# Kernel tuning notes

Hardware: AMD Instinct MI355X
Metric: run time of the kernel (lower is better)

## Reference

```python
import jax, jax.numpy as jnp
import numpy as np

MIN_NORM = 1e-15
BALL_EPS = 1e-5  # projection margin for the Poincare ball


def _tanh(x):
    return jnp.tanh(jnp.clip(x, -15.0, 15.0))


def _artanh(x):
    return jnp.arctanh(jnp.clip(x, -1.0 + 1e-5, 1.0 - 1e-5))


def givens_rotations(r, x):
    # r, x: (N, d) with d even -> (N, d)
    g = r.reshape(r.shape[0], -1, 2)
    g = g / jnp.maximum(jnp.linalg.norm(g, axis=-1, keepdims=True), MIN_NORM)
    xp = x.reshape(x.shape[0], -1, 2)
    swap = jnp.concatenate([-xp[..., 1:], xp[..., :1]], axis=-1)
    return (g[..., :1] * xp + g[..., 1:] * swap).reshape(r.shape[0], -1)


def givens_reflection(r, x):
    g = r.reshape(r.shape[0], -1, 2)
    g = g / jnp.maximum(jnp.linalg.norm(g, axis=-1, keepdims=True), MIN_NORM)
    xp = x.reshape(x.shape[0], -1, 2)
    a = jnp.concatenate([xp[..., :1], -xp[..., 1:]], axis=-1)
    b = jnp.concatenate([xp[..., 1:], xp[..., :1]], axis=-1)
    return (g[..., :1] * a + g[..., 1:] * b).reshape(r.shape[0], -1)


def expmap0(u, c):
    sqrt_c = jnp.sqrt(c)
    u_norm = jnp.maximum(jnp.linalg.norm(u, axis=-1, keepdims=True), MIN_NORM)
    return _tanh(sqrt_c * u_norm) * u / (sqrt_c * u_norm)


def mobius_add(x, y, c):
    x2 = jnp.sum(x * x, -1, keepdims=True)
    y2 = jnp.sum(y * y, -1, keepdims=True)
    xy = jnp.sum(x * y, -1, keepdims=True)
    num = (1 + 2 * c * xy + c * y2) * x + (1 - c * x2) * y
    denom = 1 + 2 * c * xy + c * c * x2 * y2
    return num / jnp.maximum(denom, MIN_NORM)


def project(x, c):
    norm = jnp.maximum(jnp.linalg.norm(x, axis=-1, keepdims=True), MIN_NORM)
    maxnorm = (1.0 - BALL_EPS) / jnp.sqrt(c)
    return jnp.where(norm > maxnorm, x / norm * maxnorm, x)


def hyp_distance_multi_c_bmm(x, v, c):
    # x: (nc, cs, d) queries; v: (nc, ns, d) candidates; c: (nc, cs, 1) curvatures
    sqrt_c = jnp.sqrt(c)                                              # (nc, cs, 1)
    vnorm = jnp.linalg.norm(v, axis=-1, keepdims=True).transpose(0, 2, 1)  # (nc, 1, ns)
    xv = jnp.einsum('bcd,bnd->bcn', x, v) / vnorm                     # (nc, cs, ns)
    gamma = _tanh(sqrt_c * vnorm) / sqrt_c                            # (nc, cs, ns)
    x2 = jnp.sum(x * x, -1, keepdims=True)                            # (nc, cs, 1)
    c1 = 1 - 2 * c * gamma * xv + c * gamma ** 2
    c2 = 1 - c * x2
    num = jnp.sqrt(jnp.maximum(c1 ** 2 * x2 + c2 ** 2 * gamma ** 2 - 2 * c1 * c2 * gamma * xv, 0.0))
    denom = 1 - 2 * c * gamma * xv + c ** 2 * gamma ** 2 * x2
    dist = _artanh(sqrt_c * num / jnp.maximum(denom, MIN_NORM))
    return 2 * dist / sqrt_c                                          # (nc, cs, ns)


def setup_inputs() -> dict:
    key = jax.random.key(0)
    nc, cs, ns, d = 16, 1024, 1024, 512
    B = nc * cs
    ks = jax.random.split(key, 8)
    return {
        'head': jax.random.normal(ks[0], (B, d), jnp.float32),
        'head_bias': jax.random.normal(ks[1], (B, 1), jnp.float32),
        'rel': jax.random.normal(ks[2], (B, d), jnp.float32),
        'rel_diag': jax.random.normal(ks[3], (B, 2 * d), jnp.float32),
        'curvature': jax.random.normal(ks[4], (B, 1), jnp.float32),
        'context': jax.random.normal(ks[5], (B, d), jnp.float32),
        'scale': jnp.full((1,), 1.0 / np.sqrt(d), jnp.float32),
        'tail': jax.random.normal(ks[6], (nc * ns, d), jnp.float32),
        'tail_bias': jax.random.normal(ks[7], (nc * ns, 1), jnp.float32),
        'chunk_size': cs,
        'neg_sample_size': ns,
    }


def reference(head, head_bias, rel, rel_diag, curvature, context, scale, tail,
              tail_bias, chunk_size, neg_sample_size):
    num_chunk = head.shape[0] // chunk_size
    d = head.shape[-1]
    c = jax.nn.softplus(curvature)                                    # (B, 1)
    rot_mat, ref_mat = jnp.split(rel_diag, 2, axis=-1)
    rot_q = givens_rotations(rot_mat, head)[:, None, :]               # (B, 1, d)
    ref_q = givens_reflection(ref_mat, head)[:, None, :]              # (B, 1, d)
    cands = jnp.concatenate([ref_q, rot_q], axis=1)                   # (B, 2, d)
    att_w = jax.nn.softmax(
        jnp.sum(context[:, None, :] * cands * scale, -1, keepdims=True), axis=1)
    att_q = jnp.sum(att_w * cands, axis=1)                            # (B, d)
    lhs = expmap0(att_q, c)
    rel_h = expmap0(rel, c)
    res = project(mobius_add(lhs, rel_h, c), c)                       # (B, d)
    x = res.reshape(num_chunk, chunk_size, d)
    v = tail.reshape(num_chunk, neg_sample_size, d)
    c3 = c.reshape(num_chunk, chunk_size, 1)
    dist = hyp_distance_multi_c_bmm(x, v, c3)                         # (nc, cs, ns)
    score = (-dist ** 2
             + head_bias.reshape(num_chunk, chunk_size, 1)
             + tail_bias.reshape(num_chunk, 1, neg_sample_size))
    return score
```

## Files before the change

kernel.cpp:

```cpp
#include <hip/hip_runtime.h>
#include <math.h>

#define DEV static __device__ __forceinline__

constexpr float MIN_NORM = 1e-15f;
constexpr float BALL_EPS = 1e-5f;
constexpr int D = 512;

typedef float f32x4 __attribute__((ext_vector_type(4)));
typedef short short8v __attribute__((ext_vector_type(8)));
typedef unsigned short ushort8v __attribute__((ext_vector_type(8)));

DEV float wave_sum(float v) {
#pragma unroll
    for (int o = 32; o > 0; o >>= 1) v += __shfl_xor(v, o, 64);
    return v;
}

DEV float tanh_clip(float x) {
    x = fminf(fmaxf(x, -15.0f), 15.0f);
    return tanhf(x);
}

DEV unsigned short f2bf(float f) {
    unsigned int u = __float_as_uint(f);
    u = (u + 0x7FFFu + ((u >> 16) & 1u)) >> 16;
    return (unsigned short)u;
}
DEV float bf2f(unsigned short h) { return __uint_as_float(((unsigned int)h) << 16); }

__global__ __launch_bounds__(64)
void preprocess_kernel(const float* __restrict__ head,
                       const float* __restrict__ rel,
                       const float* __restrict__ rel_diag,
                       const float* __restrict__ curvature,
                       const float* __restrict__ context,
                       const float* __restrict__ scale_p,
                       unsigned short* __restrict__ Ah,
                       unsigned short* __restrict__ Al,
                       float* __restrict__ row_x2,
                       float* __restrict__ row_c,
                       float* __restrict__ row_sc)
{
    const int row  = blockIdx.x;
    const int lane = threadIdx.x;
    const int base = lane * 8;
    const size_t roff = (size_t)row * D;
    const size_t doff = (size_t)row * 2 * D;

    float hv[8], rv[8], gv[8], fv[8], cxv[8];
    *(float4*)&hv[0]  = *(const float4*)(head + roff + base);
    *(float4*)&hv[4]  = *(const float4*)(head + roff + base + 4);
    *(float4*)&rv[0]  = *(const float4*)(rel + roff + base);
    *(float4*)&rv[4]  = *(const float4*)(rel + roff + base + 4);
    *(float4*)&gv[0]  = *(const float4*)(rel_diag + doff + base);
    *(float4*)&gv[4]  = *(const float4*)(rel_diag + doff + base + 4);
    *(float4*)&fv[0]  = *(const float4*)(rel_diag + doff + D + base);
    *(float4*)&fv[4]  = *(const float4*)(rel_diag + doff + D + base + 4);
    *(float4*)&cxv[0] = *(const float4*)(context + roff + base);
    *(float4*)&cxv[4] = *(const float4*)(context + roff + base + 4);

    float rq[8], rf[8];
#pragma unroll
    for (int p = 0; p < 4; ++p) {
        const float x0 = hv[2*p], x1 = hv[2*p+1];
        float g0 = gv[2*p], g1 = gv[2*p+1];
        const float gn = fmaxf(sqrtf(g0*g0 + g1*g1), MIN_NORM);
        g0 /= gn; g1 /= gn;
        rq[2*p]   = g0*x0 - g1*x1;
        rq[2*p+1] = g0*x1 + g1*x0;
        float f0 = fv[2*p], f1 = fv[2*p+1];
        const float fn = fmaxf(sqrtf(f0*f0 + f1*f1), MIN_NORM);
        f0 /= fn; f1 /= fn;
        rf[2*p]   = f0*x0 + f1*x1;
        rf[2*p+1] = f1*x0 - f0*x1;
    }

    float s0=0,s1=0,s2=0,s3=0,s4=0,s5=0,s6=0,s7=0;
#pragma unroll
    for (int e = 0; e < 8; ++e) {
        s0 += cxv[e]*rf[e];   s1 += cxv[e]*rq[e];
        s2 += rv[e]*rv[e];    s3 += rf[e]*rv[e];
        s4 += rq[e]*rv[e];    s5 += rf[e]*rf[e];
        s6 += rq[e]*rq[e];    s7 += rf[e]*rq[e];
    }
    s0 = wave_sum(s0); s1 = wave_sum(s1); s2 = wave_sum(s2); s3 = wave_sum(s3);
    s4 = wave_sum(s4); s5 = wave_sum(s5); s6 = wave_sum(s6); s7 = wave_sum(s7);

    const float cu = curvature[row];
    const float c  = fmaxf(cu, 0.0f) + log1pf(expf(-fabsf(cu)));
    const float sqc = sqrtf(c);
    const float sc  = scale_p[0];

    const float a0 = s0 * sc, a1 = s1 * sc;
    const float mx = fmaxf(a0, a1);
    const float e0 = expf(a0 - mx), e1 = expf(a1 - mx);
    const float w0 = e0 / (e0 + e1);
    const float w1 = 1.0f - w0;

    const float att2    = fmaxf(w0*w0*s5 + 2.0f*w0*w1*s7 + w1*w1*s6, 0.0f);
    const float attdrel = w0*s3 + w1*s4;
    const float u_att = fmaxf(sqrtf(att2), MIN_NORM);
    const float u_rel = fmaxf(sqrtf(s2), MIN_NORM);

    const float kl = tanh_clip(sqc * u_att) / (sqc * u_att);
    const float kr = tanh_clip(sqc * u_rel) / (sqc * u_rel);

    const float x2 = kl*kl*att2;
    const float y2 = kr*kr*s2;
    const float xy = kl*kr*attdrel;

    const float Am  = 1.0f + 2.0f*c*xy + c*y2;
    const float Bm  = 1.0f - c*x2;
    const float den = fmaxf(1.0f + 2.0f*c*xy + c*c*x2*y2, MIN_NORM);
    const float inv_den = 1.0f / den;

    float pre[8];
    float r2p = 0.0f;
#pragma unroll
    for (int e = 0; e < 8; ++e) {
        const float attq = w0*rf[e] + w1*rq[e];
        pre[e] = (Am*kl*attq + Bm*kr*rv[e]) * inv_den;
        r2p += pre[e]*pre[e];
    }
    r2p = wave_sum(r2p);

    const float nrm  = fmaxf(sqrtf(r2p), MIN_NORM);
    const float maxn = (1.0f - BALL_EPS) / sqc;
    const float psc  = (nrm > maxn) ? (maxn / nrm) : 1.0f;

    ushort8v hi, lo;
#pragma unroll
    for (int e = 0; e < 8; ++e) {
        const float o = pre[e] * psc;
        const unsigned short hb_ = f2bf(o);
        hi[e] = hb_;
        lo[e] = f2bf(o - bf2f(hb_));
    }
    *(ushort8v*)(Ah + roff + base) = hi;
    *(ushort8v*)(Al + roff + base) = lo;

    if (lane == 0) {
        row_x2[row] = r2p * psc * psc;
        row_c[row]  = c;
        row_sc[row] = sqc;
    }
}

__global__ __launch_bounds__(64)
void tailprep_kernel(const float* __restrict__ tail,
                     unsigned short* __restrict__ Bh,
                     unsigned short* __restrict__ Bl,
                     float* __restrict__ vnorm)
{
    const int row  = blockIdx.x;
    const int lane = threadIdx.x;
    const size_t roff = (size_t)row * D + lane * 8;
    float v[8];
    *(float4*)&v[0] = *(const float4*)(tail + roff);
    *(float4*)&v[4] = *(const float4*)(tail + roff + 4);
    float s = 0.0f;
    ushort8v hi, lo;
#pragma unroll
    for (int e = 0; e < 8; ++e) {
        s += v[e]*v[e];
        const unsigned short hb_ = f2bf(v[e]);
        hi[e] = hb_;
        lo[e] = f2bf(v[e] - bf2f(hb_));
    }
    s = wave_sum(s);
    *(ushort8v*)(Bh + roff) = hi;
    *(ushort8v*)(Bl + roff) = lo;
    if (lane == 0) vnorm[row] = sqrtf(s);
}

__global__ __launch_bounds__(256)
void score_kernel(const unsigned short* __restrict__ Ah,
                  const unsigned short* __restrict__ Al,
                  const unsigned short* __restrict__ Bh,
                  const unsigned short* __restrict__ Bl,
                  const float* __restrict__ vnorm,
                  const float* __restrict__ row_x2,
                  const float* __restrict__ row_c,
                  const float* __restrict__ row_sc,
                  const float* __restrict__ head_bias,
                  const float* __restrict__ tail_bias,
                  float* __restrict__ out,
                  int cs, int ns)
{
    __shared__ __align__(16) char smem[32768];

    const int bz = blockIdx.z;
    const int m0 = blockIdx.y * 128;
    const int n0 = blockIdx.x * 128;
    const int tid  = threadIdx.x;
    const int lane = tid & 63;
    const int w    = tid >> 6;
    const int wr   = w >> 1, wc = w & 1;
    const int lrow = lane & 15, lg = lane >> 4;

    f32x4 acc[4][4];
#pragma unroll
    for (int i = 0; i < 4; ++i)
#pragma unroll
        for (int j = 0; j < 4; ++j) acc[i][j] = f32x4{0.f, 0.f, 0.f, 0.f};

    const size_t Aoff = (size_t)(bz * cs + m0) * D;
    const size_t Boff = (size_t)(bz * ns + n0) * D;

    for (int p = 0; p < 3; ++p) {
        const unsigned short* Ag = ((p == 2) ? Al : Ah) + Aoff;
        const unsigned short* Bg = ((p == 1) ? Bl : Bh) + Boff;
        for (int k0 = 0; k0 < D; k0 += 64) {
#pragma unroll
            for (int it = 0; it < 4; ++it) {
                const int L = it * 256 + tid;
                const int r = L >> 3, c = L & 7;
                const int kc = c ^ (r & 7);
                __builtin_amdgcn_global_load_lds(
                    (const __attribute__((address_space(1))) unsigned int*)(Ag + (size_t)r * D + k0 + kc * 8),
                    (__attribute__((address_space(3))) unsigned int*)(smem + L * 16),
                    16, 0, 0);
            }
#pragma unroll
            for (int it = 0; it < 4; ++it) {
                const int L = it * 256 + tid;
                const int r = L >> 3, c = L & 7;
                const int kc = c ^ (r & 7);
                __builtin_amdgcn_global_load_lds(
                    (const __attribute__((address_space(1))) unsigned int*)(Bg + (size_t)r * D + k0 + kc * 8),
                    (__attribute__((address_space(3))) unsigned int*)(smem + 16384 + L * 16),
                    16, 0, 0);
            }
            __syncthreads();

#pragma unroll
            for (int kk = 0; kk < 2; ++kk) {
                short8v af[4], bfr[4];
#pragma unroll
                for (int i = 0; i < 4; ++i) {
                    const int row = wr * 64 + i * 16 + lrow;
                    const int ch  = (kk * 4 + lg) ^ (lrow & 7);
                    af[i] = *(const short8v*)(smem + row * 128 + ch * 16);
                }
#pragma unroll
                for (int j = 0; j < 4; ++j) {
                    const int row = wc * 64 + j * 16 + lrow;
                    const int ch  = (kk * 4 + lg) ^ (lrow & 7);
                    bfr[j] = *(const short8v*)(smem + 16384 + row * 128 + ch * 16);
                }
#pragma unroll
                for (int i = 0; i < 4; ++i)
#pragma unroll
                    for (int j = 0; j < 4; ++j)
                        acc[i][j] = __builtin_amdgcn_mfma_f32_16x16x32_bf16(
                            af[i], bfr[j], acc[i][j], 0, 0, 0);
            }
            __syncthreads();
        }
    }

    const int nbase = n0 + wc * 64 + lrow;
    float rvn[4], vnv[4], tb[4];
#pragma unroll
    for (int j = 0; j < 4; ++j) {
        const int gn = bz * ns + nbase + j * 16;
        const float vn = vnorm[gn];
        vnv[j] = vn;
        rvn[j] = 1.0f / vn;
        tb[j]  = tail_bias[gn];
    }
#pragma unroll
    for (int i = 0; i < 4; ++i) {
#pragma unroll
        for (int q = 0; q < 4; ++q) {
            const int gm = bz * cs + m0 + wr * 64 + i * 16 + lg * 4 + q;
            const float x2  = row_x2[gm];
            const float cc  = row_c[gm];
            const float scq = row_sc[gm];
            const float hb  = head_bias[gm];
            const float rscq = 1.0f / scq;
            float* orow = out + (size_t)gm * ns + nbase;
#pragma unroll
            for (int j = 0; j < 4; ++j) {
                const float xv = acc[i][j][q] * rvn[j];
                float xx = fminf(scq * vnv[j], 15.0f);
                const float ey = __expf(2.0f * xx);
                const float g  = (1.0f - 2.0f / (ey + 1.0f)) * rscq;
                const float c1 = 1.0f - 2.0f*cc*g*xv + cc*g*g;
                const float c2 = 1.0f - cc*x2;
                const float num = sqrtf(fmaxf(c1*c1*x2 + c2*c2*g*g - 2.0f*c1*c2*g*xv, 0.0f));
                const float den = fmaxf(1.0f - 2.0f*cc*g*xv + cc*cc*g*g*x2, MIN_NORM);
                float t = scq * num * __builtin_amdgcn_rcpf(den);
                t = fminf(t, 1.0f - 1e-5f);
                const float ath = 0.5f * __logf((1.0f + t) * __builtin_amdgcn_rcpf(1.0f - t));
                const float dist = 2.0f * rscq * ath;
                orow[j * 16] = -dist * dist + hb + tb[j];
            }
        }
    }
}

extern "C" void kernel_launch(void* const* d_in, const int* in_sizes, int n_in,
                              void* d_out, int out_size, void* d_ws, size_t ws_size,
                              hipStream_t stream)
{
    const float* head      = (const float*)d_in[0];
    const float* head_bias = (const float*)d_in[1];
    const float* rel       = (const float*)d_in[2];
    const float* rel_diag  = (const float*)d_in[3];
    const float* curvature = (const float*)d_in[4];
    const float* context   = (const float*)d_in[5];
    const float* scale     = (const float*)d_in[6];
    const float* tail      = (const float*)d_in[7];
    const float* tail_bias = (const float*)d_in[8];

    const int B  = in_sizes[1];
    const int T  = in_sizes[8];
    const int ns = out_size / B;
    const int nc = T / ns;
    const int cs = B / nc;

    unsigned short* Ah = (unsigned short*)d_ws;
    unsigned short* Al = Ah + (size_t)B * D;
    unsigned short* Bh = Al + (size_t)B * D;
    unsigned short* Bl = Bh + (size_t)T * D;
    float* row_x2 = (float*)(Bl + (size_t)T * D);
    float* row_c  = row_x2 + B;
    float* row_sc = row_c + B;
    float* vnormb = row_sc + B;

    preprocess_kernel<<<B, 64, 0, stream>>>(head, rel, rel_diag, curvature, context,
                                            scale, Ah, Al, row_x2, row_c, row_sc);
    tailprep_kernel<<<T, 64, 0, stream>>>(tail, Bh, Bl, vnormb);

    dim3 grid(ns / 128, cs / 128, nc);
    score_kernel<<<grid, 256, 0, stream>>>(Ah, Al, Bh, Bl, vnormb, row_x2, row_c, row_sc,
                                           head_bias, tail_bias, (float*)d_out, cs, ns);
}
```

Baseline: 154.0 us.

## Fuse three split-bf16 GEMM passes into a single K loop with hi/lo tiles

The three separate passes over K (Ah·Bh, Ah·Bl, Al·Bh) are merged into one loop. Each 32-wide K step loads the hi and lo halves of A and B into the same shared-memory tile and issues all three MFMAs per fragment pair. This reads A and B once instead of three times and cuts the number of loop iterations and barriers. In exchange, each global load picks its source with a per-lane select, and there are more barriers per unit of K.

```diff
diff --git a/kernel.cpp b/kernel.cpp
--- a/kernel.cpp
+++ b/kernel.cpp
@@ -208,56 +208,60 @@
     const size_t Aoff = (size_t)(bz * cs + m0) * D;
     const size_t Boff = (size_t)(bz * ns + n0) * D;
 
-    for (int p = 0; p < 3; ++p) {
-        const unsigned short* Ag = ((p == 2) ? Al : Ah) + Aoff;
-        const unsigned short* Bg = ((p == 1) ? Bl : Bh) + Boff;
-        for (int k0 = 0; k0 < D; k0 += 64) {
-#pragma unroll
-            for (int it = 0; it < 4; ++it) {
-                const int L = it * 256 + tid;
-                const int r = L >> 3, c = L & 7;
-                const int kc = c ^ (r & 7);
-                __builtin_amdgcn_global_load_lds(
-                    (const __attribute__((address_space(1))) unsigned int*)(Ag + (size_t)r * D + k0 + kc * 8),
-                    (__attribute__((address_space(3))) unsigned int*)(smem + L * 16),
-                    16, 0, 0);
+    for (int k0 = 0; k0 < D; k0 += 32) {
+#pragma unroll
+        for (int it = 0; it < 4; ++it) {
+            const int L = it * 256 + tid;
+            const int r = L >> 3, s = L & 7;
+            const int kc = s ^ (r & 7);
+            const unsigned short* src = (kc < 4)
+                ? Ah + Aoff + (size_t)r * D + k0 + kc * 8
+                : Al + Aoff + (size_t)r * D + k0 + (kc - 4) * 8;
+            __builtin_amdgcn_global_load_lds(
+                (const __attribute__((address_space(1))) unsigned int*)src,
+                (__attribute__((address_space(3))) unsigned int*)(smem + L * 16),
+                16, 0, 0);
+        }
+#pragma unroll
+        for (int it = 0; it < 4; ++it) {
+            const int L = it * 256 + tid;
+            const int r = L >> 3, s = L & 7;
+            const int kc = s ^ (r & 7);
+            const unsigned short* src = (kc < 4)
+                ? Bh + Boff + (size_t)r * D + k0 + kc * 8
+                : Bl + Boff + (size_t)r * D + k0 + (kc - 4) * 8;
+            __builtin_amdgcn_global_load_lds(
+                (const __attribute__((address_space(1))) unsigned int*)src,
+                (__attribute__((address_space(3))) unsigned int*)(smem + 16384 + L * 16),
+                16, 0, 0);
+        }
+        __syncthreads();
+
+        short8v ah[4], al[4], bh[4], bl[4];
+#pragma unroll
+        for (int i = 0; i < 4; ++i) {
+            const int r = wr * 64 + i * 16 + lrow;
+            const char* rowp = smem + r * 128;
+            ah[i] = *(const short8v*)(rowp + ((lg    ) ^ (r & 7)) * 16);
+            al[i] = *(const short8v*)(rowp + ((lg + 4) ^ (r & 7)) * 16);
+        }
+#pragma unroll
+        for (int j = 0; j < 4; ++j) {
+            const int r = wc * 64 + j * 16 + lrow;
+            const char* rowp = smem + 16384 + r * 128;
+            bh[j] = *(const short8v*)(rowp + ((lg    ) ^ (r & 7)) * 16);
+            bl[j] = *(const short8v*)(rowp + ((lg + 4) ^ (r & 7)) * 16);
+        }
+
+#pragma unroll
+        for (int i = 0; i < 4; ++i)
+#pragma unroll
+            for (int j = 0; j < 4; ++j) {
+                acc[i][j] = __builtin_amdgcn_mfma_f32_16x16x32_bf16(ah[i], bh[j], acc[i][j], 0, 0, 0);
+                acc[i][j] = __builtin_amdgcn_mfma_f32_16x16x32_bf16(ah[i], bl[j], acc[i][j], 0, 0, 0);
+                acc[i][j] = __builtin_amdgcn_mfma_f32_16x16x32_bf16(al[i], bh[j], acc[i][j], 0, 0, 0);
             }
-#pragma unroll
-            for (int it = 0; it < 4; ++it) {
-                const int L = it * 256 + tid;
-                const int r = L >> 3, c = L & 7;
-                const int kc = c ^ (r & 7);
-                __builtin_amdgcn_global_load_lds(
-                    (const __attribute__((address_space(1))) unsigned int*)(Bg + (size_t)r * D + k0 + kc * 8),
-                    (__attribute__((address_space(3))) unsigned int*)(smem + 16384 + L * 16),
-                    16, 0, 0);
-            }
-            __syncthreads();
-
-#pragma unroll
-            for (int kk = 0; kk < 2; ++kk) {
-                short8v af[4], bfr[4];
-#pragma unroll
-                for (int i = 0; i < 4; ++i) {
-                    const int row = wr * 64 + i * 16 + lrow;
-                    const int ch  = (kk * 4 + lg) ^ (lrow & 7);
-                    af[i] = *(const short8v*)(smem + row * 128 + ch * 16);
-                }
-#pragma unroll
-                for (int j = 0; j < 4; ++j) {
-                    const int row = wc * 64 + j * 16 + lrow;
-                    const int ch  = (kk * 4 + lg) ^ (lrow & 7);
-                    bfr[j] = *(const short8v*)(smem + 16384 + row * 128 + ch * 16);
-                }
-#pragma unroll
-                for (int i = 0; i < 4; ++i)
-#pragma unroll
-                    for (int j = 0; j < 4; ++j)
-                        acc[i][j] = __builtin_amdgcn_mfma_f32_16x16x32_bf16(
-                            af[i], bfr[j], acc[i][j], 0, 0, 0);
-            }
-            __syncthreads();
-        }
+        __syncthreads();
     }
 
     const int nbase = n0 + wc * 64 + lrow;
```

After: 148.5 us. -3.6%, faster.

## Restructure score GEMM into 256x256 double-buffered tiles with fused hi/lo split-bf16 passes

Applied to the files above, without the earlier changes.

The score GEMM moves from 128x128 tiles with 256 threads to 256x256 tiles with 512 threads and 128KB of dynamic LDS. Each staged panel now holds both the hi and lo bf16 halves, so the three split-precision products run in one K sweep instead of three separate passes. The LDS buffers are double-buffered, with the next panel's loads overlapped against the MFMA phases, and s_setprio plus barriers interleave the waves. The aim is more data reuse, fewer reloads of A/B and hidden global latency. The cost is more registers, one block per CU, and fewer blocks in the grid, which can hurt occupancy and tail balance. The grid also now requires cs and ns to be multiples of 256.

```diff
diff --git a/kernel.cpp b/kernel.cpp
--- a/kernel.cpp
+++ b/kernel.cpp
@@ -174,7 +174,7 @@
     if (lane == 0) vnorm[row] = sqrtf(s);
 }
 
-__global__ __launch_bounds__(256)
+__global__ __launch_bounds__(512, 2)
 void score_kernel(const unsigned short* __restrict__ Ah,
                   const unsigned short* __restrict__ Al,
                   const unsigned short* __restrict__ Bh,
@@ -188,79 +188,121 @@
                   float* __restrict__ out,
                   int cs, int ns)
 {
-    __shared__ __align__(16) char smem[32768];
+    extern __shared__ __align__(16) char smem[];
 
     const int bz = blockIdx.z;
-    const int m0 = blockIdx.y * 128;
-    const int n0 = blockIdx.x * 128;
+    const int m0 = blockIdx.y * 256;
+    const int n0 = blockIdx.x * 256;
     const int tid  = threadIdx.x;
     const int lane = tid & 63;
     const int w    = tid >> 6;
-    const int wr   = w >> 1, wc = w & 1;
+    const int wr   = w >> 2, wn = w & 3;
     const int lrow = lane & 15, lg = lane >> 4;
 
-    f32x4 acc[4][4];
-#pragma unroll
-    for (int i = 0; i < 4; ++i)
+    f32x4 acc[8][4];
+#pragma unroll
+    for (int i = 0; i < 8; ++i)
 #pragma unroll
         for (int j = 0; j < 4; ++j) acc[i][j] = f32x4{0.f, 0.f, 0.f, 0.f};
 
     const size_t Aoff = (size_t)(bz * cs + m0) * D;
     const size_t Boff = (size_t)(bz * ns + n0) * D;
 
-    for (int p = 0; p < 3; ++p) {
-        const unsigned short* Ag = ((p == 2) ? Al : Ah) + Aoff;
-        const unsigned short* Bg = ((p == 1) ? Bl : Bh) + Boff;
-        for (int k0 = 0; k0 < D; k0 += 64) {
-#pragma unroll
-            for (int it = 0; it < 4; ++it) {
-                const int L = it * 256 + tid;
-                const int r = L >> 3, c = L & 7;
-                const int kc = c ^ (r & 7);
-                __builtin_amdgcn_global_load_lds(
-                    (const __attribute__((address_space(1))) unsigned int*)(Ag + (size_t)r * D + k0 + kc * 8),
-                    (__attribute__((address_space(3))) unsigned int*)(smem + L * 16),
-                    16, 0, 0);
-            }
-#pragma unroll
-            for (int it = 0; it < 4; ++it) {
-                const int L = it * 256 + tid;
-                const int r = L >> 3, c = L & 7;
-                const int kc = c ^ (r & 7);
-                __builtin_amdgcn_global_load_lds(
-                    (const __attribute__((address_space(1))) unsigned int*)(Bg + (size_t)r * D + k0 + kc * 8),
-                    (__attribute__((address_space(3))) unsigned int*)(smem + 16384 + L * 16),
-                    16, 0, 0);
-            }
-            __syncthreads();
-
-#pragma unroll
-            for (int kk = 0; kk < 2; ++kk) {
-                short8v af[4], bfr[4];
-#pragma unroll
-                for (int i = 0; i < 4; ++i) {
-                    const int row = wr * 64 + i * 16 + lrow;
-                    const int ch  = (kk * 4 + lg) ^ (lrow & 7);
-                    af[i] = *(const short8v*)(smem + row * 128 + ch * 16);
-                }
-#pragma unroll
-                for (int j = 0; j < 4; ++j) {
-                    const int row = wc * 64 + j * 16 + lrow;
-                    const int ch  = (kk * 4 + lg) ^ (lrow & 7);
-                    bfr[j] = *(const short8v*)(smem + 16384 + row * 128 + ch * 16);
-                }
-#pragma unroll
-                for (int i = 0; i < 4; ++i)
-#pragma unroll
-                    for (int j = 0; j < 4; ++j)
-                        acc[i][j] = __builtin_amdgcn_mfma_f32_16x16x32_bf16(
-                            af[i], bfr[j], acc[i][j], 0, 0, 0);
-            }
-            __syncthreads();
+#define STAGE_PANEL(dstbase, Hi, Lo, Goff, K0)                                     \
+    do {                                                                           \
+        _Pragma("unroll")                                                          \
+        for (int it_ = 0; it_ < 4; ++it_) {                                        \
+            const int L_ = it_ * 512 + tid;                                        \
+            const int r_ = L_ >> 3, s_ = L_ & 7;                                   \
+            const int kc_ = s_ ^ (r_ & 7);                                         \
+            const unsigned short* src_ = (kc_ < 4)                                 \
+                ? Hi + Goff + (size_t)r_ * D + (K0) + kc_ * 8                      \
+                : Lo + Goff + (size_t)r_ * D + (K0) + (kc_ - 4) * 8;               \
+            __builtin_amdgcn_global_load_lds(                                      \
+                (const __attribute__((address_space(1))) unsigned int*)src_,       \
+                (__attribute__((address_space(3))) unsigned int*)((dstbase) + L_ * 16), \
+                16, 0, 0);                                                         \
+        }                                                                          \
+    } while (0)
+
+#define READ_A(M, AH_, AL_)                                                        \
+    do {                                                                           \
+        const int r_ = wr * 128 + (M) * 16 + lrow;                                 \
+        const char* rp_ = curb + r_ * 128;                                         \
+        AH_ = *(const short8v*)(rp_ + ((lg    ) ^ (r_ & 7)) * 16);                 \
+        AL_ = *(const short8v*)(rp_ + ((lg + 4) ^ (r_ & 7)) * 16);                 \
+    } while (0)
+
+#define MFMA_(A_, B_, C_) __builtin_amdgcn_mfma_f32_16x16x32_bf16(A_, B_, C_, 0, 0, 0)
+
+#define TRIPROD(M0, M1)                                                            \
+    do {                                                                           \
+        _Pragma("unroll") for (int n = 0; n < 4; ++n) acc[M0][n] = MFMA_(ah0, bh[n], acc[M0][n]); \
+        _Pragma("unroll") for (int n = 0; n < 4; ++n) acc[M1][n] = MFMA_(ah1, bh[n], acc[M1][n]); \
+        _Pragma("unroll") for (int n = 0; n < 4; ++n) acc[M0][n] = MFMA_(ah0, bl[n], acc[M0][n]); \
+        _Pragma("unroll") for (int n = 0; n < 4; ++n) acc[M1][n] = MFMA_(ah1, bl[n], acc[M1][n]); \
+        _Pragma("unroll") for (int n = 0; n < 4; ++n) acc[M0][n] = MFMA_(al0, bh[n], acc[M0][n]); \
+        _Pragma("unroll") for (int n = 0; n < 4; ++n) acc[M1][n] = MFMA_(al1, bh[n], acc[M1][n]); \
+    } while (0)
+
+    STAGE_PANEL(smem, Ah, Al, Aoff, 0);
+    STAGE_PANEL(smem + 32768, Bh, Bl, Boff, 0);
+    __syncthreads();
+
+#pragma unroll 1
+    for (int t = 0; t < 16; ++t) {
+        char* curb = smem + (t & 1) * 65536;
+        char* nxtb = smem + ((t + 1) & 1) * 65536;
+        const int k0n = (t + 1) * 32;
+        const bool more = (t < 15);
+
+        short8v bh[4], bl[4];
+        short8v ah0, al0, ah1, al1;
+
+        if (more) STAGE_PANEL(nxtb, Ah, Al, Aoff, k0n);
+#pragma unroll
+        for (int n = 0; n < 4; ++n) {
+            const int r_ = wn * 64 + n * 16 + lrow;
+            const char* rp_ = curb + 32768 + r_ * 128;
+            bh[n] = *(const short8v*)(rp_ + ((lg    ) ^ (r_ & 7)) * 16);
+            bl[n] = *(const short8v*)(rp_ + ((lg + 4) ^ (r_ & 7)) * 16);
         }
-    }
-
-    const int nbase = n0 + wc * 64 + lrow;
+        READ_A(0, ah0, al0);
+        READ_A(1, ah1, al1);
+        __builtin_amdgcn_s_barrier();
+        __builtin_amdgcn_s_setprio(1);
+        TRIPROD(0, 1);
+        __builtin_amdgcn_s_setprio(0);
+        __builtin_amdgcn_s_barrier();
+
+        if (more) STAGE_PANEL(nxtb + 32768, Bh, Bl, Boff, k0n);
+        READ_A(2, ah0, al0);
+        READ_A(3, ah1, al1);
+        __builtin_amdgcn_s_barrier();
+        __builtin_amdgcn_s_setprio(1);
+        TRIPROD(2, 3);
+        __builtin_amdgcn_s_setprio(0);
+        __builtin_amdgcn_s_barrier();
+
+        READ_A(4, ah0, al0);
+        READ_A(5, ah1, al1);
+        __builtin_amdgcn_s_barrier();
+        __builtin_amdgcn_s_setprio(1);
+        TRIPROD(4, 5);
+        __builtin_amdgcn_s_setprio(0);
+        __builtin_amdgcn_s_barrier();
+
+        READ_A(6, ah0, al0);
+        READ_A(7, ah1, al1);
+        __builtin_amdgcn_s_barrier();
+        __builtin_amdgcn_s_setprio(1);
+        TRIPROD(6, 7);
+        __builtin_amdgcn_s_setprio(0);
+
+        __syncthreads();
+    }
+
+    const int nbase = n0 + wn * 64 + lrow;
     float rvn[4], vnv[4], tb[4];
 #pragma unroll
     for (int j = 0; j < 4; ++j) {
@@ -271,10 +313,10 @@
         tb[j]  = tail_bias[gn];
     }
 #pragma unroll
-    for (int i = 0; i < 4; ++i) {
+    for (int i = 0; i < 8; ++i) {
 #pragma unroll
         for (int q = 0; q < 4; ++q) {
-            const int gm = bz * cs + m0 + wr * 64 + i * 16 + lg * 4 + q;
+            const int gm = bz * cs + m0 + wr * 128 + i * 16 + lg * 4 + q;
             const float x2  = row_x2[gm];
             const float cc  = row_c[gm];
             const float scq = row_sc[gm];
@@ -299,6 +341,10 @@
             }
         }
     }
+#undef STAGE_PANEL
+#undef READ_A
+#undef MFMA_
+#undef TRIPROD
 }
 
 extern "C" void kernel_launch(void* const* d_in, const int* in_sizes, int n_in,
@@ -334,7 +380,10 @@
                                             scale, Ah, Al, row_x2, row_c, row_sc);
     tailprep_kernel<<<T, 64, 0, stream>>>(tail, Bh, Bl, vnormb);
 
-    dim3 grid(ns / 128, cs / 128, nc);
-    score_kernel<<<grid, 256, 0, stream>>>(Ah, Al, Bh, Bl, vnormb, row_x2, row_c, row_sc,
-                                           head_bias, tail_bias, (float*)d_out, cs, ns);
-}
+    (void)hipFuncSetAttribute((const void*)score_kernel,
+                              hipFuncAttributeMaxDynamicSharedMemorySize, 131072);
+    dim3 grid(ns / 256, cs / 256, nc);
+    score_kernel<<<grid, 512, 131072, stream>>>(Ah, Al, Bh, Bl, vnormb, row_x2, row_c,
+                                                row_sc, head_bias, tail_bias,
+                                                (float*)d_out, cs, ns);
+}
```

Result: faster. 145.7 us (-5.4%).
